# Performance work log

Hardware: AMD Instinct MI355X
Metric: run time of the kernel (lower is better)

Reference implementation:

```python
import jax, jax.numpy as jnp
import numpy as np

B, T, V, E, H = 4096, 16, 512, 512, 1024


def setup_inputs() -> dict:
    key = jax.random.key(0)
    ks = jax.random.split(key, 8)
    s = 0.05  # weight init scale
    return {
        "encoded_input": jax.random.normal(ks[0], (B, H), jnp.float32),
        "target": jax.random.randint(ks[1], (B, T), 0, V, jnp.int32),
        "emb": jax.random.normal(ks[2], (V, E), jnp.float32) * s,
        "W_ih": jax.random.normal(ks[3], (4 * H, E), jnp.float32) * s,
        "W_hh": jax.random.normal(ks[4], (4 * H, H), jnp.float32) * s,
        "b_ih": jax.random.normal(ks[5], (4 * H,), jnp.float32) * s,
        "b_hh": jax.random.normal(ks[6], (4 * H,), jnp.float32) * s,
        "W_out": jax.random.normal(ks[7], (V, H), jnp.float32) * s,
    }


def reference(encoded_input, target, emb, W_ih, W_hh, b_ih, b_hh, W_out):
    # Teacher-forced char LSTM decoder. Dropout(0.1) is identity in eval mode.
    b, t = target.shape
    # input char ids: start token 0, then shifted targets
    inp_ids = jnp.concatenate(
        [jnp.zeros((b, 1), target.dtype), target[:, :-1]], axis=1)  # [B,T]
    x = emb[inp_ids]  # [B,T,E]
    # precompute input contribution to gates for all steps
    xg = jnp.einsum('bte,ge->btg', x, W_ih) + b_ih + b_hh  # [B,T,4H]

    def step(carry, xs):
        h, c = carry
        xg_t, tgt_t = xs  # [B,4H], [B]
        gates = xg_t + h @ W_hh.T  # [B,4H]
        i, f, g, o = jnp.split(gates, 4, axis=-1)  # torch order i,f,g,o
        i = jax.nn.sigmoid(i)
        f = jax.nn.sigmoid(f)
        g = jnp.tanh(g)
        o = jax.nn.sigmoid(o)
        c = f * c + i * g
        h = o * jnp.tanh(c)
        logits = h @ W_out.T  # [B,V]
        # NLL of log_softmax at target index, expressed stably
        lse = jax.nn.logsumexp(logits, axis=-1)
        tgt_logit = jnp.take_along_axis(logits, tgt_t[:, None], axis=1)[:, 0]
        loss_t = lse - tgt_logit  # [B]
        return (h, c), loss_t

    h0 = encoded_input  # hidden = (encoded, encoded) for 1 layer
    (_, _), losses = jax.lax.scan(
        step, (h0, h0),
        (jnp.swapaxes(xg, 0, 1), target.T))  # scan over time: [T,B,...]
    return losses.sum(axis=0) / t  # [B] per-example mean loss
```

## Files before the change

### kernel.cpp

```cpp
#include <hip/hip_runtime.h>
#include <hip/hip_bf16.h>
#include <stdint.h>

typedef __attribute__((ext_vector_type(8))) short bf16x8;
typedef __attribute__((ext_vector_type(4))) float f32x4;

#define DEV __device__ __forceinline__

static constexpr int Bn = 4096;
static constexpr int Tn = 16;
static constexpr int Vn = 512;
static constexpr int En = 512;
static constexpr int Hn = 1024;
static constexpr int G4 = 4096;
static constexpr int KX = En + Hn;

DEV unsigned short f2bf(float f) {
    union { float f; uint32_t u; } v; v.f = f;
    return (unsigned short)((v.u + 0x7fffu + ((v.u >> 16) & 1u)) >> 16);
}
DEV float bf2f(unsigned short h) {
    union { uint32_t u; float f; } v; v.u = (uint32_t)h << 16; return v.f;
}
DEV float sigmoidf_(float x) { return 1.f / (1.f + __expf(-x)); }
DEV float tanhf_(float x)    { return 1.f - 2.f / (1.f + __expf(2.f * x)); }

DEV bf16x8 cvt8(const float* p) {
    f32x4 a = *(const f32x4*)p;
    f32x4 b = *(const f32x4*)(p + 4);
    bf16x8 o;
    o[0] = (short)f2bf(a[0]); o[1] = (short)f2bf(a[1]);
    o[2] = (short)f2bf(a[2]); o[3] = (short)f2bf(a[3]);
    o[4] = (short)f2bf(b[0]); o[5] = (short)f2bf(b[1]);
    o[6] = (short)f2bf(b[2]); o[7] = (short)f2bf(b[3]);
    return o;
}

template <int BM, int BN, int EPI>
__launch_bounds__(256, 2)
__global__ void gemm_k(const unsigned short* __restrict__ A, int lda,
                       const unsigned short* __restrict__ Bw, int ldb,
                       int K,
                       const float* __restrict__ biasp,
                       const float* __restrict__ EGb,
                       const int* __restrict__ target, int t,
                       float* __restrict__ CstF,
                       unsigned short* __restrict__ Hout,
                       float* __restrict__ Out,
                       unsigned short* __restrict__ Outb, int ldo)
{
    constexpr int BK = 32;
    constexpr int WM = BM / 2, WN = BN / 2;
    constexpr int MI = WM / 16, NJ = WN / 16;
    constexpr int SHSTR = 40;

    __shared__ __align__(16) unsigned short sA[BM * BK];
    __shared__ __align__(16) unsigned short sB[BN * BK];
    __shared__ __align__(16) unsigned short sH[(EPI == 1) ? 128 * SHSTR : 1];

    const int tid = threadIdx.x;
    const int l   = tid & 63;
    const int w   = tid >> 6;
    const int wm  = w >> 1, wn = w & 1;
    const int m0  = blockIdx.y * BM;
    const int n0  = blockIdx.x * BN;

    f32x4 acc[MI][NJ];
#pragma unroll
    for (int i = 0; i < MI; i++)
#pragma unroll
        for (int j = 0; j < NJ; j++) acc[i][j] = f32x4{0.f, 0.f, 0.f, 0.f};

    const int srow = l >> 2;
    const int scol = (l & 3) * 8;
    const int q    = l >> 4;
    const int c15  = l & 15;

    int ids[4] = {0, 0, 0, 0};
    if constexpr (EPI == 1) {
        if (t > 0) {
#pragma unroll
            for (int j = 0; j < 4; j++) {
                int b = n0 + wn * 64 + j * 16 + c15;
                ids[j] = target[(size_t)b * Tn + (t - 1)];
            }
        }
    }

    for (int k0 = 0; k0 < K; k0 += BK) {
#pragma unroll
        for (int c = 0; c < BM / 64; c++) {
            const unsigned short* src =
                A + (size_t)(m0 + c * 64 + w * 16 + srow) * lda + k0 + scol;
            unsigned short* dst = &sA[(c * 64 + w * 16) * BK];
            __builtin_amdgcn_global_load_lds(
                (const __attribute__((address_space(1))) uint32_t*)src,
                (__attribute__((address_space(3))) uint32_t*)dst, 16, 0, 0);
        }
#pragma unroll
        for (int c = 0; c < BN / 64; c++) {
            const unsigned short* src =
                Bw + (size_t)(n0 + c * 64 + w * 16 + srow) * ldb + k0 + scol;
            unsigned short* dst = &sB[(c * 64 + w * 16) * BK];
            __builtin_amdgcn_global_load_lds(
                (const __attribute__((address_space(1))) uint32_t*)src,
                (__attribute__((address_space(3))) uint32_t*)dst, 16, 0, 0);
        }
        __syncthreads();

        bf16x8 aF[MI], bF[NJ];
#pragma unroll
        for (int i = 0; i < MI; i++)
            aF[i] = *(const bf16x8*)&sA[(wm * WM + i * 16 + c15) * BK + q * 8];
#pragma unroll
        for (int j = 0; j < NJ; j++)
            bF[j] = *(const bf16x8*)&sB[(wn * WN + j * 16 + c15) * BK + q * 8];
#pragma unroll
        for (int i = 0; i < MI; i++)
#pragma unroll
            for (int j = 0; j < NJ; j++)
                acc[i][j] = __builtin_amdgcn_mfma_f32_16x16x32_bf16(
                    aF[i], bF[j], acc[i][j], 0, 0, 0);
        __syncthreads();
    }

    if constexpr (EPI == 1) {
        const int bx = blockIdx.x, by = blockIdx.y;
#pragma unroll
        for (int i = 0; i < 4; i++) {
            const int U = by * 32 + wm * 16 + i * 4 + q;
#pragma unroll
            for (int j = 0; j < 4; j++) {
                f32x4 eg = *(const f32x4*)&EGb[(size_t)ids[j] * G4 + U * 4];
                float ig = sigmoidf_(acc[i][j][0] + eg[0]);
                float fg = sigmoidf_(acc[i][j][1] + eg[1]);
                float gg = tanhf_  (acc[i][j][2] + eg[2]);
                float og = sigmoidf_(acc[i][j][3] + eg[3]);
                const size_t cidx =
                    (size_t)(((by * 32 + bx) * 4 + w) * 16 + i * 4 + j) * 64 + l;
                float cOld = CstF[cidx];
                float cNew = fg * cOld + ig * gg;
                float h    = og * tanhf_(cNew);
                CstF[cidx] = cNew;
                sH[(wn * 64 + j * 16 + c15) * SHSTR + wm * 16 + i * 4 + q] =
                    f2bf(h);
            }
        }
        __syncthreads();
        {
            const int bl = tid >> 1, half = tid & 1;
            const unsigned short* s = &sH[bl * SHSTR + half * 16];
            bf16x8 v0 = *(const bf16x8*)s;
            bf16x8 v1 = *(const bf16x8*)(s + 8);
            size_t o = (size_t)(bx * 128 + bl) * Hn + by * 32 + half * 16;
            *(bf16x8*)&Hout[o]     = v0;
            *(bf16x8*)&Hout[o + 8] = v1;
        }
    } else {
#pragma unroll
        for (int j = 0; j < NJ; j++) {
            const int colp = n0 + wn * WN + j * 16 + c15;
            const float bj = biasp ? biasp[colp] : 0.f;
#pragma unroll
            for (int i = 0; i < MI; i++) {
                const size_t rb = (size_t)(m0 + wm * WM + i * 16 + 4 * q);
#pragma unroll
                for (int r = 0; r < 4; r++) {
                    float vv = acc[i][j][r] + bj;
                    if constexpr (EPI == 0) Out[(rb + r) * ldo + colp] = vv;
                    else Outb[(rb + r) * ldo + colp] = f2bf(vv);
                }
            }
        }
    }
}

__launch_bounds__(512, 4)
__global__ void logits_lse(const unsigned short* __restrict__ A,
                           const unsigned short* __restrict__ Wob,
                           const int* __restrict__ target,
                           float* __restrict__ lossT)
{
    constexpr int BK = 32;
    __shared__ __align__(16) unsigned short sA[64 * BK];
    __shared__ __align__(16) unsigned short sB[512 * BK];
    __shared__ float redS[8 * 64];
    __shared__ float redT[8 * 64];
    __shared__ int   tgL[64];

    const int tid = threadIdx.x;
    const int l   = tid & 63;
    const int w   = tid >> 6;
    const int q   = l >> 4, c15 = l & 15;
    const int ra0 = blockIdx.x * 64;

    if (tid < 64) {
        int ra = ra0 + tid;
        tgL[tid] = target[(size_t)(ra & (Bn - 1)) * Tn + (ra >> 12)];
    }

    f32x4 acc[4][4];
#pragma unroll
    for (int i = 0; i < 4; i++)
#pragma unroll
        for (int j = 0; j < 4; j++) acc[i][j] = f32x4{0.f, 0.f, 0.f, 0.f};

    const int srow = l >> 2;
    const int scol = (l & 3) * 8;

    for (int k0 = 0; k0 < Hn; k0 += BK) {
#pragma unroll
        for (int c = 0; c < 4; c++) {
            const unsigned short* src =
                Wob + (size_t)(w * 64 + c * 16 + srow) * Hn + k0 + scol;
            unsigned short* dst = &sB[(w * 64 + c * 16) * BK];
            __builtin_amdgcn_global_load_lds(
                (const __attribute__((address_space(1))) uint32_t*)src,
                (__attribute__((address_space(3))) uint32_t*)dst, 16, 0, 0);
        }
        if (w < 4) {
            const unsigned short* src =
                A + (size_t)(ra0 + w * 16 + srow) * Hn + k0 + scol;
            unsigned short* dst = &sA[(w * 16) * BK];
            __builtin_amdgcn_global_load_lds(
                (const __attribute__((address_space(1))) uint32_t*)src,
                (__attribute__((address_space(3))) uint32_t*)dst, 16, 0, 0);
        }
        __syncthreads();

        bf16x8 aF[4], bF[4];
#pragma unroll
        for (int i = 0; i < 4; i++)
            aF[i] = *(const bf16x8*)&sA[(i * 16 + c15) * BK + q * 8];
#pragma unroll
        for (int j = 0; j < 4; j++)
            bF[j] = *(const bf16x8*)&sB[(w * 64 + j * 16 + c15) * BK + q * 8];
#pragma unroll
        for (int i = 0; i < 4; i++)
#pragma unroll
            for (int j = 0; j < 4; j++)
                acc[i][j] = __builtin_amdgcn_mfma_f32_16x16x32_bf16(
                    aF[i], bF[j], acc[i][j], 0, 0, 0);
        __syncthreads();
    }

#pragma unroll
    for (int i = 0; i < 4; i++)
#pragma unroll
        for (int rr = 0; rr < 4; rr++) {
            const int rloc = i * 16 + q * 4 + rr;
            const int tg = tgL[rloc];
            float ps = 0.f, tv = 0.f;
#pragma unroll
            for (int j = 0; j < 4; j++) {
                float v = acc[i][j][rr];
                ps += __expf(v);
                int col = w * 64 + j * 16 + c15;
                tv += (col == tg) ? v : 0.f;
            }
#pragma unroll
            for (int d = 1; d < 16; d <<= 1) {
                ps += __shfl_xor(ps, d);
                tv += __shfl_xor(tv, d);
            }
            if (c15 == 0) {
                redS[w * 64 + rloc] = ps;
                redT[w * 64 + rloc] = tv;
            }
        }
    __syncthreads();
    if (tid < 64) {
        float se = 0.f, tv = 0.f;
#pragma unroll
        for (int w8 = 0; w8 < 8; w8++) {
            se += redS[w8 * 64 + tid];
            tv += redT[w8 * 64 + tid];
        }
        lossT[ra0 + tid] = __logf(se) - tv;
    }
}

__global__ void prep_w(const float* __restrict__ Wih,
                       const float* __restrict__ Whh,
                       unsigned short* __restrict__ Wp)
{
    int i = blockIdx.x * 256 + threadIdx.x;
    int n = i / 192, kc = (i % 192) * 8;
    int g = n & 3, u = n >> 2;
    const float* src = (kc < En) ? (Wih + (size_t)(g * Hn + u) * En + kc)
                                 : (Whh + (size_t)(g * Hn + u) * Hn + (kc - En));
    *(bf16x8*)&Wp[(size_t)n * KX + kc] = cvt8(src);
}

__global__ void prep_bias(const float* __restrict__ bih,
                          const float* __restrict__ bhh,
                          float* __restrict__ biasp)
{
    int n = blockIdx.x * 256 + threadIdx.x;
    int g = n & 3, u = n >> 2;
    biasp[n] = bih[g * Hn + u] + bhh[g * Hn + u];
}

__global__ void prep_wout(const float* __restrict__ Wout,
                          unsigned short* __restrict__ Wob)
{
    int i = blockIdx.x * 256 + threadIdx.x;
    size_t off = (size_t)i * 8;
    *(bf16x8*)&Wob[off] = cvt8(Wout + off);
}

__global__ void prep_emb(const float* __restrict__ emb,
                         unsigned short* __restrict__ embb)
{
    int i = blockIdx.x * 256 + threadIdx.x;
    size_t off = (size_t)i * 8;
    *(bf16x8*)&embb[off] = cvt8(emb + off);
}

__global__ void init_state(const float* __restrict__ enc,
                           float* __restrict__ CstF,
                           unsigned short* __restrict__ Xh0,
                           float* __restrict__ loss)
{
    int f = blockIdx.x * 256 + threadIdx.x;
    int l = f & 63, q = l >> 4, c15 = l & 15;
    int ij = (f >> 6) & 15, i = ij >> 2, j = ij & 3;
    int w = (f >> 10) & 3, wm = w >> 1, wn = w & 1;
    int bx = (f >> 12) & 31, by = (f >> 17) & 31;
    int mg = bx * 128 + wn * 64 + j * 16 + c15;
    int U  = by * 32 + wm * 16 + i * 4 + q;
    CstF[f] = enc[(size_t)mg * Hn + U];
    if (f < Bn * Hn / 8) {
        int m = f >> 7, u8 = (f & 127) * 8;
        *(bf16x8*)&Xh0[(size_t)m * Hn + u8] = cvt8(enc + (size_t)m * Hn + u8);
    }
    if (f < Bn) loss[f] = 0.f;
}

__global__ void lse_k(const unsigned short* __restrict__ lg,
                      const int* __restrict__ target, int t,
                      float* __restrict__ lossOut)
{
    int w = threadIdx.x >> 6, l = threadIdx.x & 63;
    int ra = blockIdx.x * 4 + w;
    const unsigned short* row = lg + (size_t)ra * Vn;
    bf16x8 v = *(const bf16x8*)&row[l * 8];
    float x0 = bf2f((unsigned short)v[0]), x1 = bf2f((unsigned short)v[1]);
    float x2 = bf2f((unsigned short)v[2]), x3 = bf2f((unsigned short)v[3]);
    float x4 = bf2f((unsigned short)v[4]), x5 = bf2f((unsigned short)v[5]);
    float x6 = bf2f((unsigned short)v[6]), x7 = bf2f((unsigned short)v[7]);
    float mx = fmaxf(fmaxf(fmaxf(x0, x1), fmaxf(x2, x3)),
                     fmaxf(fmaxf(x4, x5), fmaxf(x6, x7)));
#pragma unroll
    for (int d = 1; d < 64; d <<= 1) mx = fmaxf(mx, __shfl_xor(mx, d));
    float se = __expf(x0 - mx) + __expf(x1 - mx) + __expf(x2 - mx) +
               __expf(x3 - mx) + __expf(x4 - mx) + __expf(x5 - mx) +
               __expf(x6 - mx) + __expf(x7 - mx);
#pragma unroll
    for (int d = 1; d < 64; d <<= 1) se += __shfl_xor(se, d);
    if (l == 0) {
        int tg = target[(size_t)ra * Tn + t];
        lossOut[ra] += (mx + __logf(se)) - bf2f(row[tg]);
    }
}

__global__ void finalize_b(const float* __restrict__ lossT,
                           float* __restrict__ out)
{
    int m = blockIdx.x * 256 + threadIdx.x;
    float s = 0.f;
#pragma unroll
    for (int k = 0; k < 16; k++) s += lossT[(size_t)k * Bn + m];
    out[m] = s * (1.f / 16.f);
}

__global__ void finalize_s(const float* __restrict__ loss,
                           float* __restrict__ out)
{
    int m = blockIdx.x * 256 + threadIdx.x;
    out[m] = loss[m] * (1.f / 16.f);
}

extern "C" void kernel_launch(void* const* d_in, const int* in_sizes, int n_in,
                              void* d_out, int out_size, void* d_ws, size_t ws_size,
                              hipStream_t stream)
{
    const float* enc    = (const float*)d_in[0];
    const int*   target = (const int*)d_in[1];
    const float* emb    = (const float*)d_in[2];
    const float* Wih    = (const float*)d_in[3];
    const float* Whh    = (const float*)d_in[4];
    const float* bih    = (const float*)d_in[5];
    const float* bhh    = (const float*)d_in[6];
    const float* Wout   = (const float*)d_in[7];
    float* out = (float*)d_out;
    (void)in_sizes; (void)n_in; (void)out_size;

    constexpr size_t SZ_Wp    = (size_t)G4 * KX * 2;
    constexpr size_t SZ_Wob   = (size_t)Vn * Hn * 2;
    constexpr size_t SZ_biasp = (size_t)G4 * 4;
    constexpr size_t SZ_embb  = (size_t)Vn * En * 2;
    constexpr size_t SZ_EGb   = (size_t)Vn * G4 * 4;
    constexpr size_t SZ_Cst   = (size_t)Bn * Hn * 4;
    constexpr size_t SZ_H     = (size_t)Bn * Hn * 2;
    constexpr size_t SZ_LGS   = (size_t)Bn * Vn * 2;
    constexpr size_t SZ_LT    = (size_t)Bn * Tn * 4;
    auto pad = [](size_t b) { return (b + 255) & ~(size_t)255; };
    const size_t fixed = pad(SZ_Wp) + pad(SZ_Wob) + pad(SZ_biasp) +
                         pad(SZ_embb) + pad(SZ_EGb) + pad(SZ_Cst);
    const size_t needB = fixed + 17 * pad(SZ_H) + pad(SZ_LGS) + pad(SZ_LT);
    const bool batched = ws_size >= needB;

    size_t off = 0;
    char* base = (char*)d_ws;
    auto alloc = [&](size_t bytes) -> void* {
        void* p = base + off; off += pad(bytes); return p;
    };
    unsigned short* Wp    = (unsigned short*)alloc(SZ_Wp);
    unsigned short* Wob   = (unsigned short*)alloc(SZ_Wob);
    float*          biasp = (float*)alloc(SZ_biasp);
    unsigned short* embb  = (unsigned short*)alloc(SZ_embb);
    float*          EGb   = (float*)alloc(SZ_EGb);
    float*          CstF  = (float*)alloc(SZ_Cst);
    const int nslot = batched ? 17 : 3;
    unsigned short* Hs    = (unsigned short*)alloc((size_t)nslot * pad(SZ_H));
    unsigned short* lgS   = (unsigned short*)alloc(SZ_LGS);
    float*          lossT = (float*)alloc(batched ? SZ_LT : (size_t)Bn * 4);
    const size_t HSLOT = pad(SZ_H) / 2;

    prep_w    <<<3072, 256, 0, stream>>>(Wih, Whh, Wp);
    prep_bias <<<16,   256, 0, stream>>>(bih, bhh, biasp);
    prep_wout <<<256,  256, 0, stream>>>(Wout, Wob);
    prep_emb  <<<128,  256, 0, stream>>>(emb, embb);
    init_state<<<16384, 256, 0, stream>>>(enc, CstF, Hs, lossT);

    gemm_k<128, 128, 0><<<dim3(32, 4), 256, 0, stream>>>(
        embb, En, Wp, KX, En, biasp, nullptr, nullptr, 0,
        nullptr, nullptr, EGb, nullptr, G4);

    for (int t = 0; t < Tn; t++) {
        unsigned short* hIn  = Hs + (size_t)(batched ? t : (t % 3)) * HSLOT;
        unsigned short* hOut = Hs + (size_t)(batched ? (t + 1) : ((t + 1) % 3)) * HSLOT;
        gemm_k<128, 128, 1><<<dim3(32, 32), 256, 0, stream>>>(
            Wp + En, KX, hIn, Hn, Hn, nullptr, EGb, target, t,
            CstF, hOut, nullptr, nullptr, 0);
        if (!batched) {
            gemm_k<128, 64, 2><<<dim3(8, 32), 256, 0, stream>>>(
                hOut, Hn, Wob, Hn, Hn, nullptr, nullptr, nullptr, 0,
                nullptr, nullptr, nullptr, lgS, Vn);
            lse_k<<<1024, 256, 0, stream>>>(lgS, target, t, lossT);
        }
    }

    if (batched) {
        logits_lse<<<1024, 512, 0, stream>>>(
            Hs + HSLOT, Wob, target, lossT);
        finalize_b<<<16, 256, 0, stream>>>(lossT, out);
    } else {
        finalize_s<<<16, 256, 0, stream>>>(lossT, out);
    }
}
```

Baseline: 1.004 ms.

## Replace recurrent gate GEMM with 256x256-tiled double-buffered swizzled LSTM kernel

```diff
diff --git a/kernel.cpp b/kernel.cpp
--- a/kernel.cpp
+++ b/kernel.cpp
@@ -6,6 +6,7 @@
 typedef __attribute__((ext_vector_type(4))) float f32x4;
 
 #define DEV __device__ __forceinline__
+#define MFMA16(a, b, c) __builtin_amdgcn_mfma_f32_16x16x32_bf16(a, b, c, 0, 0, 0)
 
 static constexpr int Bn = 4096;
 static constexpr int Tn = 16;
@@ -36,27 +37,174 @@
     return o;
 }
 
+__launch_bounds__(512, 2)
+__global__ void lstm8(const unsigned short* __restrict__ Whp8,
+                      const unsigned short* __restrict__ Hin,
+                      const float* __restrict__ EGb,
+                      const int* __restrict__ target, int t,
+                      float* __restrict__ CstF,
+                      unsigned short* __restrict__ Hout)
+{
+    __shared__ __align__(16) unsigned short lds[65536];
+
+    const int tid = threadIdx.x;
+    const int l   = tid & 63;
+    const int w   = tid >> 6;
+    const int wm  = w >> 2, wn = w & 3;
+    const int q   = l >> 4, c15 = l & 15;
+    const int bx  = blockIdx.x, by = blockIdx.y;
+    const int n0  = bx * 256;
+
+    const int cB = (((l & 7) ^ (l >> 3)) << 3);
+
+    const int sw0   = ((q ^ (c15 & 7)) << 3);
+    const int offA0 = c15 * 64 + sw0;
+    const int offB0 = ((wn & 1) * 64 + c15) * 64 + sw0;
+
+    f32x4 acc[8][4];
+#pragma unroll
+    for (int i = 0; i < 8; i++)
+#pragma unroll
+        for (int j = 0; j < 4; j++) acc[i][j] = f32x4{0.f, 0.f, 0.f, 0.f};
+
+    auto stageA = [&](int kts, int cbuf) {
+        const unsigned short* page =
+            Whp8 + (((size_t)(by * 16 + kts) * 2) << 13);
+#pragma unroll
+        for (int h = 0; h < 2; h++)
+#pragma unroll
+            for (int L = 0; L < 2; L++) {
+                const unsigned short* src =
+                    page + h * 8192 + L * 4096 + w * 512 + l * 8;
+                unsigned short* dst =
+                    &lds[cbuf * 16384 + h * 8192 + L * 4096 + w * 512];
+                __builtin_amdgcn_global_load_lds(
+                    (const __attribute__((address_space(1))) uint32_t*)src,
+                    (__attribute__((address_space(3))) uint32_t*)dst, 16, 0, 0);
+            }
+    };
+    auto stageB = [&](int kts, int cbuf) {
+#pragma unroll
+        for (int h = 0; h < 2; h++)
+#pragma unroll
+            for (int L = 0; L < 2; L++) {
+                const unsigned short* src =
+                    Hin + (size_t)(n0 + h * 128 + L * 64 + w * 8 + (l >> 3)) * Hn
+                        + kts * 64 + cB;
+                unsigned short* dst =
+                    &lds[32768 + cbuf * 16384 + h * 8192 + L * 4096 + w * 512];
+                __builtin_amdgcn_global_load_lds(
+                    (const __attribute__((address_space(1))) uint32_t*)src,
+                    (__attribute__((address_space(3))) uint32_t*)dst, 16, 0, 0);
+            }
+    };
+
+    stageA(0, 0); stageB(0, 0);
+    stageA(1, 1); stageB(1, 1);
+    asm volatile("s_waitcnt vmcnt(8)" ::: "memory");
+    __builtin_amdgcn_s_barrier();
+
+#pragma unroll 2
+    for (int kt = 0; kt < 16; kt++) {
+        const int cur = kt & 1;
+        const unsigned short* Ab = &lds[cur * 16384 + wm * 8192];
+        const unsigned short* Bb = &lds[32768 + cur * 16384 + (wn >> 1) * 8192];
+        bf16x8 aF[8], bF[4];
+
+#pragma unroll
+        for (int i = 0; i < 8; i++)
+            aF[i] = *(const bf16x8*)&Ab[offA0 + i * 1024];
+#pragma unroll
+        for (int j = 0; j < 4; j++)
+            bF[j] = *(const bf16x8*)&Bb[offB0 + j * 1024];
+        __builtin_amdgcn_s_setprio(1);
+#pragma unroll
+        for (int i = 0; i < 8; i++)
+#pragma unroll
+            for (int j = 0; j < 4; j++)
+                acc[i][j] = MFMA16(aF[i], bF[j], acc[i][j]);
+        __builtin_amdgcn_s_setprio(0);
+
+#pragma unroll
+        for (int i = 0; i < 8; i++)
+            aF[i] = *(const bf16x8*)&Ab[(offA0 ^ 32) + i * 1024];
+#pragma unroll
+        for (int j = 0; j < 4; j++)
+            bF[j] = *(const bf16x8*)&Bb[(offB0 ^ 32) + j * 1024];
+        __builtin_amdgcn_s_setprio(1);
+#pragma unroll
+        for (int i = 0; i < 8; i++)
+#pragma unroll
+            for (int j = 0; j < 4; j++)
+                acc[i][j] = MFMA16(aF[i], bF[j], acc[i][j]);
+        __builtin_amdgcn_s_setprio(0);
+        __builtin_amdgcn_s_barrier();
+
+        const int kts = (kt + 2 < 16) ? (kt + 2) : 15;
+        stageA(kts, cur);
+        stageB(kts, cur);
+        asm volatile("s_waitcnt vmcnt(8)" ::: "memory");
+        __builtin_amdgcn_s_barrier();
+    }
+
+    int ids[4];
+#pragma unroll
+    for (int j = 0; j < 4; j++)
+        ids[j] = (t > 0)
+            ? target[(size_t)(n0 + wn * 64 + j * 16 + c15) * Tn + (t - 1)] : 0;
+
+    const int U0 = by * 64;
+    unsigned short* sH = &lds[32768];
+#pragma unroll
+    for (int i = 0; i < 8; i++) {
+        const int Uloc = wm * 32 + i * 4 + q;
+#pragma unroll
+        for (int j = 0; j < 4; j++) {
+            f32x4 eg = *(const f32x4*)&EGb[(size_t)ids[j] * G4 + (U0 + Uloc) * 4];
+            float ig = sigmoidf_(acc[i][j][0] + eg[0]);
+            float fg = sigmoidf_(acc[i][j][1] + eg[1]);
+            float gg = tanhf_  (acc[i][j][2] + eg[2]);
+            float og = sigmoidf_(acc[i][j][3] + eg[3]);
+            const size_t cidx =
+                ((((size_t)(by * 16 + bx) * 8 + w) * 32 + i * 4 + j) << 6) + l;
+            float cOld = CstF[cidx];
+            float cNew = fg * cOld + ig * gg;
+            float h    = og * tanhf_(cNew);
+            CstF[cidx] = cNew;
+            const int bl = wn * 64 + j * 16 + c15;
+            sH[bl * 64 + (Uloc ^ ((bl & 7) << 3))] = f2bf(h);
+        }
+    }
+    __builtin_amdgcn_s_barrier();
+    {
+        const int row = tid >> 1;
+        const int hs  = tid & 1;
+        const int sx  = row & 7;
+        size_t go = (size_t)(n0 + row) * Hn + U0 + hs * 32;
+#pragma unroll
+        for (int s = 0; s < 4; s++) {
+            const int slog = hs * 4 + s;
+            bf16x8 v = *(const bf16x8*)&sH[row * 64 + ((slog ^ sx) << 3)];
+            *(bf16x8*)&Hout[go + s * 8] = v;
+        }
+    }
+}
+
 template <int BM, int BN, int EPI>
 __launch_bounds__(256, 2)
 __global__ void gemm_k(const unsigned short* __restrict__ A, int lda,
                        const unsigned short* __restrict__ Bw, int ldb,
                        int K,
                        const float* __restrict__ biasp,
-                       const float* __restrict__ EGb,
-                       const int* __restrict__ target, int t,
-                       float* __restrict__ CstF,
-                       unsigned short* __restrict__ Hout,
                        float* __restrict__ Out,
                        unsigned short* __restrict__ Outb, int ldo)
 {
     constexpr int BK = 32;
     constexpr int WM = BM / 2, WN = BN / 2;
     constexpr int MI = WM / 16, NJ = WN / 16;
-    constexpr int SHSTR = 40;
 
     __shared__ __align__(16) unsigned short sA[BM * BK];
     __shared__ __align__(16) unsigned short sB[BN * BK];
-    __shared__ __align__(16) unsigned short sH[(EPI == 1) ? 128 * SHSTR : 1];
 
     const int tid = threadIdx.x;
     const int l   = tid & 63;
@@ -75,17 +223,6 @@
     const int scol = (l & 3) * 8;
     const int q    = l >> 4;
     const int c15  = l & 15;
-
-    int ids[4] = {0, 0, 0, 0};
-    if constexpr (EPI == 1) {
-        if (t > 0) {
-#pragma unroll
-            for (int j = 0; j < 4; j++) {
-                int b = n0 + wn * 64 + j * 16 + c15;
-                ids[j] = target[(size_t)b * Tn + (t - 1)];
-            }
-        }
-    }
 
     for (int k0 = 0; k0 < K; k0 += BK) {
 #pragma unroll
@@ -119,57 +256,22 @@
         for (int i = 0; i < MI; i++)
 #pragma unroll
             for (int j = 0; j < NJ; j++)
-                acc[i][j] = __builtin_amdgcn_mfma_f32_16x16x32_bf16(
-                    aF[i], bF[j], acc[i][j], 0, 0, 0);
+                acc[i][j] = MFMA16(aF[i], bF[j], acc[i][j]);
         __syncthreads();
     }
 
-    if constexpr (EPI == 1) {
-        const int bx = blockIdx.x, by = blockIdx.y;
-#pragma unroll
-        for (int i = 0; i < 4; i++) {
-            const int U = by * 32 + wm * 16 + i * 4 + q;
-#pragma unroll
-            for (int j = 0; j < 4; j++) {
-                f32x4 eg = *(const f32x4*)&EGb[(size_t)ids[j] * G4 + U * 4];
-                float ig = sigmoidf_(acc[i][j][0] + eg[0]);
-                float fg = sigmoidf_(acc[i][j][1] + eg[1]);
-                float gg = tanhf_  (acc[i][j][2] + eg[2]);
-                float og = sigmoidf_(acc[i][j][3] + eg[3]);
-                const size_t cidx =
-                    (size_t)(((by * 32 + bx) * 4 + w) * 16 + i * 4 + j) * 64 + l;
-                float cOld = CstF[cidx];
-                float cNew = fg * cOld + ig * gg;
-                float h    = og * tanhf_(cNew);
-                CstF[cidx] = cNew;
-                sH[(wn * 64 + j * 16 + c15) * SHSTR + wm * 16 + i * 4 + q] =
-                    f2bf(h);
-            }
-        }
-        __syncthreads();
-        {
-            const int bl = tid >> 1, half = tid & 1;
-            const unsigned short* s = &sH[bl * SHSTR + half * 16];
-            bf16x8 v0 = *(const bf16x8*)s;
-            bf16x8 v1 = *(const bf16x8*)(s + 8);
-            size_t o = (size_t)(bx * 128 + bl) * Hn + by * 32 + half * 16;
-            *(bf16x8*)&Hout[o]     = v0;
-            *(bf16x8*)&Hout[o + 8] = v1;
-        }
-    } else {
-#pragma unroll
-        for (int j = 0; j < NJ; j++) {
-            const int colp = n0 + wn * WN + j * 16 + c15;
-            const float bj = biasp ? biasp[colp] : 0.f;
-#pragma unroll
-            for (int i = 0; i < MI; i++) {
-                const size_t rb = (size_t)(m0 + wm * WM + i * 16 + 4 * q);
-#pragma unroll
-                for (int r = 0; r < 4; r++) {
-                    float vv = acc[i][j][r] + bj;
-                    if constexpr (EPI == 0) Out[(rb + r) * ldo + colp] = vv;
-                    else Outb[(rb + r) * ldo + colp] = f2bf(vv);
-                }
+#pragma unroll
+    for (int j = 0; j < NJ; j++) {
+        const int colp = n0 + wn * WN + j * 16 + c15;
+        const float bj = biasp ? biasp[colp] : 0.f;
+#pragma unroll
+        for (int i = 0; i < MI; i++) {
+            const size_t rb = (size_t)(m0 + wm * WM + i * 16 + 4 * q);
+#pragma unroll
+            for (int r = 0; r < 4; r++) {
+                float vv = acc[i][j][r] + bj;
+                if constexpr (EPI == 0) Out[(rb + r) * ldo + colp] = vv;
+                else Outb[(rb + r) * ldo + colp] = f2bf(vv);
             }
         }
     }
@@ -239,8 +341,7 @@
         for (int i = 0; i < 4; i++)
 #pragma unroll
             for (int j = 0; j < 4; j++)
-                acc[i][j] = __builtin_amdgcn_mfma_f32_16x16x32_bf16(
-                    aF[i], bF[j], acc[i][j], 0, 0, 0);
+                acc[i][j] = MFMA16(aF[i], bF[j], acc[i][j]);
         __syncthreads();
     }
 
@@ -292,6 +393,23 @@
     *(bf16x8*)&Wp[(size_t)n * KX + kc] = cvt8(src);
 }
 
+__global__ void prep_w8(const float* __restrict__ Whh,
+                        unsigned short* __restrict__ Whp8)
+{
+    int idx = blockIdx.x * 256 + threadIdx.x;
+    int o = idx * 8;
+    int p = o & 8191;
+    int h = (o >> 13) & 1;
+    int kt = (o >> 14) & 15;
+    int by = o >> 18;
+    int r = p >> 6;
+    int slot = (p & 63) >> 3;
+    int cl = ((slot ^ (r & 7)) << 3);
+    int n = by * 256 + h * 128 + r;
+    int g = n & 3, u = n >> 2;
+    *(bf16x8*)&Whp8[o] = cvt8(Whh + (size_t)(g * Hn + u) * Hn + kt * 64 + cl);
+}
+
 __global__ void prep_bias(const float* __restrict__ bih,
                           const float* __restrict__ bhh,
                           float* __restrict__ biasp)
@@ -324,12 +442,12 @@
 {
     int f = blockIdx.x * 256 + threadIdx.x;
     int l = f & 63, q = l >> 4, c15 = l & 15;
-    int ij = (f >> 6) & 15, i = ij >> 2, j = ij & 3;
-    int w = (f >> 10) & 3, wm = w >> 1, wn = w & 1;
-    int bx = (f >> 12) & 31, by = (f >> 17) & 31;
-    int mg = bx * 128 + wn * 64 + j * 16 + c15;
-    int U  = by * 32 + wm * 16 + i * 4 + q;
-    CstF[f] = enc[(size_t)mg * Hn + U];
+    int ij = (f >> 6) & 31, i = ij >> 2, j = ij & 3;
+    int w = (f >> 11) & 7, wm = w >> 2, wn = w & 3;
+    int bx = (f >> 14) & 15, by = (f >> 18) & 15;
+    int b = bx * 256 + wn * 64 + j * 16 + c15;
+    int U = by * 64 + wm * 32 + i * 4 + q;
+    CstF[f] = enc[(size_t)b * Hn + U];
     if (f < Bn * Hn / 8) {
         int m = f >> 7, u8 = (f & 127) * 8;
         *(bf16x8*)&Xh0[(size_t)m * Hn + u8] = cvt8(enc + (size_t)m * Hn + u8);
@@ -397,6 +515,7 @@
     (void)in_sizes; (void)n_in; (void)out_size;
 
     constexpr size_t SZ_Wp    = (size_t)G4 * KX * 2;
+    constexpr size_t SZ_Whp8  = (size_t)G4 * Hn * 2;
     constexpr size_t SZ_Wob   = (size_t)Vn * Hn * 2;
     constexpr size_t SZ_biasp = (size_t)G4 * 4;
     constexpr size_t SZ_embb  = (size_t)Vn * En * 2;
@@ -406,8 +525,8 @@
     constexpr size_t SZ_LGS   = (size_t)Bn * Vn * 2;
     constexpr size_t SZ_LT    = (size_t)Bn * Tn * 4;
     auto pad = [](size_t b) { return (b + 255) & ~(size_t)255; };
-    const size_t fixed = pad(SZ_Wp) + pad(SZ_Wob) + pad(SZ_biasp) +
-                         pad(SZ_embb) + pad(SZ_EGb) + pad(SZ_Cst);
+    const size_t fixed = pad(SZ_Wp) + pad(SZ_Whp8) + pad(SZ_Wob) +
+                         pad(SZ_biasp) + pad(SZ_embb) + pad(SZ_EGb) + pad(SZ_Cst);
     const size_t needB = fixed + 17 * pad(SZ_H) + pad(SZ_LGS) + pad(SZ_LT);
     const bool batched = ws_size >= needB;
 
@@ -417,6 +536,7 @@
         void* p = base + off; off += pad(bytes); return p;
     };
     unsigned short* Wp    = (unsigned short*)alloc(SZ_Wp);
+    unsigned short* Whp8  = (unsigned short*)alloc(SZ_Whp8);
     unsigned short* Wob   = (unsigned short*)alloc(SZ_Wob);
     float*          biasp = (float*)alloc(SZ_biasp);
     unsigned short* embb  = (unsigned short*)alloc(SZ_embb);
@@ -429,32 +549,29 @@
     const size_t HSLOT = pad(SZ_H) / 2;
 
     prep_w    <<<3072, 256, 0, stream>>>(Wih, Whh, Wp);
+    prep_w8   <<<2048, 256, 0, stream>>>(Whh, Whp8);
     prep_bias <<<16,   256, 0, stream>>>(bih, bhh, biasp);
     prep_wout <<<256,  256, 0, stream>>>(Wout, Wob);
     prep_emb  <<<128,  256, 0, stream>>>(emb, embb);
     init_state<<<16384, 256, 0, stream>>>(enc, CstF, Hs, lossT);
 
     gemm_k<128, 128, 0><<<dim3(32, 4), 256, 0, stream>>>(
-        embb, En, Wp, KX, En, biasp, nullptr, nullptr, 0,
-        nullptr, nullptr, EGb, nullptr, G4);
+        embb, En, Wp, KX, En, biasp, EGb, nullptr, G4);
 
     for (int t = 0; t < Tn; t++) {
         unsigned short* hIn  = Hs + (size_t)(batched ? t : (t % 3)) * HSLOT;
         unsigned short* hOut = Hs + (size_t)(batched ? (t + 1) : ((t + 1) % 3)) * HSLOT;
-        gemm_k<128, 128, 1><<<dim3(32, 32), 256, 0, stream>>>(
-            Wp + En, KX, hIn, Hn, Hn, nullptr, EGb, target, t,
-            CstF, hOut, nullptr, nullptr, 0);
+        lstm8<<<dim3(16, 16), 512, 0, stream>>>(
+            Whp8, hIn, EGb, target, t, CstF, hOut);
         if (!batched) {
             gemm_k<128, 64, 2><<<dim3(8, 32), 256, 0, stream>>>(
-                hOut, Hn, Wob, Hn, Hn, nullptr, nullptr, nullptr, 0,
-                nullptr, nullptr, nullptr, lgS, Vn);
+                hOut, Hn, Wob, Hn, Hn, nullptr, nullptr, lgS, Vn);
             lse_k<<<1024, 256, 0, stream>>>(lgS, target, t, lossT);
         }
     }
 
     if (batched) {
-        logits_lse<<<1024, 512, 0, stream>>>(
-            Hs + HSLOT, Wob, target, lossT);
+        logits_lse<<<1024, 512, 0, stream>>>(Hs + HSLOT, Wob, target, lossT);
         finalize_b<<<16, 256, 0, stream>>>(lossT, out);
     } else {
         finalize_s<<<16, 256, 0, stream>>>(lossT, out);
```

After: 900.2 us. -10.3%, faster.
